# Performance work log

Hardware: AMD Instinct MI355X
Metric: run time of the kernel (lower is better)

The kernel has to match this reference:

```python
import jax, jax.numpy as jnp
import numpy as np
import math

N = 262144   # total points
D = 256      # FEATURE_DIM
B = 16       # batch_size (scenes)

def setup_inputs() -> dict:
    key = jax.random.key(0)
    k0, k1, k2, k3 = jax.random.split(key, 4)
    point_features = jax.random.normal(k0, (N, D), dtype=jnp.float32)
    point_cls_scores = jax.random.uniform(k1, (N,), dtype=jnp.float32)
    # column 0 = sorted batch index in [0, B); remaining columns unused by forward
    bidx = jnp.sort(jax.random.randint(k2, (N,), 0, B, dtype=jnp.int32))
    rest = jax.random.randint(k2, (N, 3), 0, B, dtype=jnp.int32)
    point_coords = jnp.concatenate([bidx[:, None], rest], axis=1)
    # kaiming_uniform_ on (1, D): bound = sqrt(6 / fan_in) with a=sqrt(5) default -> kaiming_uniform_ (no a arg) uses a=0: bound = sqrt(6/D)
    bound = math.sqrt(6.0 / D)
    fc_weight = jax.random.uniform(k3, (1, D), dtype=jnp.float32, minval=-bound, maxval=bound)
    fc_bias = jnp.zeros((1,), dtype=jnp.float32)
    return {
        "point_features": point_features,
        "point_cls_scores": point_cls_scores,
        "point_coords": point_coords,
        "fc_weight": fc_weight,
        "fc_bias": fc_bias,
        "batch_size": B,
    }

def reference(point_features, point_cls_scores, point_coords, fc_weight, fc_bias, batch_size):
    seg = point_coords[:, 0]                                   # [N] int batch ids
    pf = point_features * point_cls_scores[:, None]            # [N, D] scaled features
    sums = jax.ops.segment_sum(pf, seg, num_segments=batch_size)            # [B, D]
    counts = jax.ops.segment_sum(jnp.ones((pf.shape[0],), pf.dtype), seg,
                                 num_segments=batch_size)                   # [B]
    scene_feature = sums / counts[:, None]                     # per-scene mean, [B, D]
    domainness = jax.nn.sigmoid(scene_feature @ fc_weight.T + fc_bias)      # [B, 1]
    return domainness
```

## Files before the change

kernel.cpp:

```cpp
#include <hip/hip_runtime.h>
#include <math.h>

#define NPTS 262144
#define DIM 256
#define NB 16

#define BLOCKS 2048
#define THREADS 256
#define RPB 128
#define WAVES 4
#define ITERS (RPB / WAVES)

__global__ __launch_bounds__(THREADS) void seg_reduce_kernel(
    const float* __restrict__ pf,
    const float* __restrict__ scores,
    const int*   __restrict__ coords,
    float* __restrict__ sums,
    float* __restrict__ counts)
{
    __shared__ float s_score[RPB];
    __shared__ int   s_batch[RPB];
    __shared__ float s_part[WAVES][DIM];

    const int t    = threadIdx.x;
    const int lane = t & 63;
    const int wid  = t >> 6;
    const int col4 = lane << 2;
    const int row0 = blockIdx.x * RPB;

    if (t < RPB) {
        s_score[t] = scores[row0 + t];
        s_batch[t] = coords[(size_t)(row0 + t) * 4];
    }
    __syncthreads();

    const float* base = pf + (size_t)row0 * DIM + col4;

    if (s_batch[0] == s_batch[RPB - 1]) {
        float a0 = 0.f, a1 = 0.f, a2 = 0.f, a3 = 0.f;
        #pragma unroll 8
        for (int it = 0; it < ITERS; ++it) {
            const int r   = (it << 2) + wid;
            const float s = s_score[r];
            const float4 f = *reinterpret_cast<const float4*>(base + (size_t)r * DIM);
            a0 = fmaf(s, f.x, a0);
            a1 = fmaf(s, f.y, a1);
            a2 = fmaf(s, f.z, a2);
            a3 = fmaf(s, f.w, a3);
        }
        float4* dstp = reinterpret_cast<float4*>(&s_part[wid][col4]);
        *dstp = make_float4(a0, a1, a2, a3);
        __syncthreads();
        const int b0 = s_batch[0];
        const float v = s_part[0][t] + s_part[1][t] + s_part[2][t] + s_part[3][t];
        atomicAdd(&sums[(size_t)b0 * DIM + t], v);
        if (t == 0) atomicAdd(&counts[b0], (float)RPB);
    } else {
        float a0 = 0.f, a1 = 0.f, a2 = 0.f, a3 = 0.f;
        float cnt = 0.f;
        int cur_b = -1;
        for (int it = 0; it < ITERS; ++it) {
            const int r   = (it << 2) + wid;
            const int b   = s_batch[r];
            const float s = s_score[r];
            if (b != cur_b) {
                if (cur_b >= 0) {
                    float* dst = sums + (size_t)cur_b * DIM + col4;
                    atomicAdd(dst + 0, a0);
                    atomicAdd(dst + 1, a1);
                    atomicAdd(dst + 2, a2);
                    atomicAdd(dst + 3, a3);
                    if (lane == 0) atomicAdd(counts + cur_b, cnt);
                }
                a0 = a1 = a2 = a3 = 0.f;
                cnt = 0.f;
                cur_b = b;
            }
            const float4 f = *reinterpret_cast<const float4*>(base + (size_t)r * DIM);
            a0 = fmaf(s, f.x, a0);
            a1 = fmaf(s, f.y, a1);
            a2 = fmaf(s, f.z, a2);
            a3 = fmaf(s, f.w, a3);
            cnt += 1.f;
        }
        if (cur_b >= 0) {
            float* dst = sums + (size_t)cur_b * DIM + col4;
            atomicAdd(dst + 0, a0);
            atomicAdd(dst + 1, a1);
            atomicAdd(dst + 2, a2);
            atomicAdd(dst + 3, a3);
            if (lane == 0) atomicAdd(counts + cur_b, cnt);
        }
    }
}

__global__ __launch_bounds__(1024) void head_kernel(
    const float* __restrict__ sums,
    const float* __restrict__ counts,
    const float* __restrict__ w,
    const float* __restrict__ bias,
    float* __restrict__ out)
{
    const int t    = threadIdx.x;
    const int b    = t >> 6;
    const int lane = t & 63;
    const int c    = lane << 2;

    const float inv = 1.f / counts[b];
    const float4 sv = *reinterpret_cast<const float4*>(sums + (size_t)b * DIM + c);
    const float4 wv = *reinterpret_cast<const float4*>(w + c);
    float p = (sv.x * wv.x + sv.y * wv.y + sv.z * wv.z + sv.w * wv.w) * inv;

    #pragma unroll
    for (int off = 32; off > 0; off >>= 1)
        p += __shfl_down(p, off, 64);

    if (lane == 0)
        out[b] = 1.f / (1.f + expf(-(p + bias[0])));
}

extern "C" void kernel_launch(void* const* d_in, const int* in_sizes, int n_in,
                              void* d_out, int out_size, void* d_ws, size_t ws_size,
                              hipStream_t stream) {
    const float* pf      = (const float*)d_in[0];
    const float* scores  = (const float*)d_in[1];
    const int*   coords  = (const int*)d_in[2];
    const float* fc_w    = (const float*)d_in[3];
    const float* fc_b    = (const float*)d_in[4];
    (void)in_sizes; (void)n_in; (void)out_size; (void)ws_size;

    float* sums   = (float*)d_ws;
    float* counts = sums + (size_t)NB * DIM;
    float* out    = (float*)d_out;

    hipMemsetAsync(d_ws, 0, (size_t)(NB * DIM + NB) * sizeof(float), stream);

    seg_reduce_kernel<<<BLOCKS, THREADS, 0, stream>>>(pf, scores, coords, sums, counts);
    head_kernel<<<1, 1024, 0, stream>>>(sums, counts, fc_w, fc_b, out);
}
```

Baseline: 373.8 us.

## Replace uniform-block atomics with per-block partials and a per-scene stage-2 reduction

Blocks whose rows all belong to one scene now write their 256-wide partial sum and scene id to a workspace buffer instead of atomically adding into a shared per-scene sum. A new stage-2 kernel, one block per scene, scans all block ids, sums the matching partials, adds the atomic results from mixed-scene blocks, and applies the linear head and sigmoid. Batch ids are no longer staged in shared memory; only the first and last row ids are loaded, and mixed blocks read coords directly. This removes contention from 2048 blocks hitting 16 rows of atomics, but adds about 2 MB of partial writes and reads plus a serial scan over 2048 ids in each stage-2 block.

```diff
diff --git a/kernel.cpp b/kernel.cpp
--- a/kernel.cpp
+++ b/kernel.cpp
@@ -5,22 +5,25 @@
 #define DIM 256
 #define NB 16
 
-#define BLOCKS 2048
+#define S1_BLOCKS 2048
 #define THREADS 256
-#define RPB 128
+#define RPB (NPTS / S1_BLOCKS)
 #define WAVES 4
 #define ITERS (RPB / WAVES)
 
-__global__ __launch_bounds__(THREADS) void seg_reduce_kernel(
+
+__global__ __launch_bounds__(THREADS) void stage1_kernel(
     const float* __restrict__ pf,
     const float* __restrict__ scores,
     const int*   __restrict__ coords,
-    float* __restrict__ sums,
-    float* __restrict__ counts)
+    float* __restrict__ partials,
+    int*   __restrict__ bids,
+    float* __restrict__ slow_sums,
+    float* __restrict__ slow_counts)
 {
     __shared__ float s_score[RPB];
-    __shared__ int   s_batch[RPB];
     __shared__ float s_part[WAVES][DIM];
+    __shared__ int   s_b0, s_b1;
 
     const int t    = threadIdx.x;
     const int lane = t & 63;
@@ -28,15 +31,14 @@
     const int col4 = lane << 2;
     const int row0 = blockIdx.x * RPB;
 
-    if (t < RPB) {
-        s_score[t] = scores[row0 + t];
-        s_batch[t] = coords[(size_t)(row0 + t) * 4];
-    }
+    if (t < RPB) s_score[t] = scores[row0 + t];
+    if (t == 0)  s_b0 = coords[(size_t)row0 * 4];
+    if (t == 1)  s_b1 = coords[(size_t)(row0 + RPB - 1) * 4];
     __syncthreads();
 
     const float* base = pf + (size_t)row0 * DIM + col4;
 
-    if (s_batch[0] == s_batch[RPB - 1]) {
+    if (s_b0 == s_b1) {
         float a0 = 0.f, a1 = 0.f, a2 = 0.f, a3 = 0.f;
         #pragma unroll 8
         for (int it = 0; it < ITERS; ++it) {
@@ -48,29 +50,28 @@
             a2 = fmaf(s, f.z, a2);
             a3 = fmaf(s, f.w, a3);
         }
-        float4* dstp = reinterpret_cast<float4*>(&s_part[wid][col4]);
-        *dstp = make_float4(a0, a1, a2, a3);
+        *reinterpret_cast<float4*>(&s_part[wid][col4]) = make_float4(a0, a1, a2, a3);
         __syncthreads();
-        const int b0 = s_batch[0];
-        const float v = s_part[0][t] + s_part[1][t] + s_part[2][t] + s_part[3][t];
-        atomicAdd(&sums[(size_t)b0 * DIM + t], v);
-        if (t == 0) atomicAdd(&counts[b0], (float)RPB);
+        partials[(size_t)blockIdx.x * DIM + t] =
+            s_part[0][t] + s_part[1][t] + s_part[2][t] + s_part[3][t];
+        if (t == 0) bids[blockIdx.x] = s_b0;
     } else {
+        if (t == 0) bids[blockIdx.x] = -1;
         float a0 = 0.f, a1 = 0.f, a2 = 0.f, a3 = 0.f;
         float cnt = 0.f;
         int cur_b = -1;
         for (int it = 0; it < ITERS; ++it) {
             const int r   = (it << 2) + wid;
-            const int b   = s_batch[r];
+            const int b   = coords[(size_t)(row0 + r) * 4];
             const float s = s_score[r];
             if (b != cur_b) {
                 if (cur_b >= 0) {
-                    float* dst = sums + (size_t)cur_b * DIM + col4;
+                    float* dst = slow_sums + (size_t)cur_b * DIM + col4;
                     atomicAdd(dst + 0, a0);
                     atomicAdd(dst + 1, a1);
                     atomicAdd(dst + 2, a2);
                     atomicAdd(dst + 3, a3);
-                    if (lane == 0) atomicAdd(counts + cur_b, cnt);
+                    if (lane == 0) atomicAdd(slow_counts + cur_b, cnt);
                 }
                 a0 = a1 = a2 = a3 = 0.f;
                 cnt = 0.f;
@@ -84,39 +85,68 @@
             cnt += 1.f;
         }
         if (cur_b >= 0) {
-            float* dst = sums + (size_t)cur_b * DIM + col4;
+            float* dst = slow_sums + (size_t)cur_b * DIM + col4;
             atomicAdd(dst + 0, a0);
             atomicAdd(dst + 1, a1);
             atomicAdd(dst + 2, a2);
             atomicAdd(dst + 3, a3);
-            if (lane == 0) atomicAdd(counts + cur_b, cnt);
+            if (lane == 0) atomicAdd(slow_counts + cur_b, cnt);
         }
     }
 }
 
-__global__ __launch_bounds__(1024) void head_kernel(
-    const float* __restrict__ sums,
-    const float* __restrict__ counts,
+__global__ __launch_bounds__(THREADS) void stage2_kernel(
+    const float* __restrict__ partials,
+    const int*   __restrict__ bids,
+    const float* __restrict__ slow_sums,
+    const float* __restrict__ slow_counts,
     const float* __restrict__ w,
     const float* __restrict__ bias,
     float* __restrict__ out)
 {
+    __shared__ int   s_bids[S1_BLOCKS];
+    __shared__ float s_part[WAVES][DIM];
+    __shared__ int   s_nm[WAVES];
+    __shared__ float s_red[WAVES];
+
+    const int b    = blockIdx.x;
     const int t    = threadIdx.x;
-    const int b    = t >> 6;
     const int lane = t & 63;
-    const int c    = lane << 2;
+    const int wid  = t >> 6;
+    const int col4 = lane << 2;
 
-    const float inv = 1.f / counts[b];
-    const float4 sv = *reinterpret_cast<const float4*>(sums + (size_t)b * DIM + c);
-    const float4 wv = *reinterpret_cast<const float4*>(w + c);
-    float p = (sv.x * wv.x + sv.y * wv.y + sv.z * wv.z + sv.w * wv.w) * inv;
+    for (int i = t; i < S1_BLOCKS; i += THREADS) s_bids[i] = bids[i];
+    __syncthreads();
 
+    float a0 = 0.f, a1 = 0.f, a2 = 0.f, a3 = 0.f;
+    int nm = 0;
+    for (int blk = wid; blk < S1_BLOCKS; blk += WAVES) {
+        if (s_bids[blk] == b) {
+            const float4 f = *reinterpret_cast<const float4*>(
+                partials + (size_t)blk * DIM + col4);
+            a0 += f.x; a1 += f.y; a2 += f.z; a3 += f.w;
+            ++nm;
+        }
+    }
+    *reinterpret_cast<float4*>(&s_part[wid][col4]) = make_float4(a0, a1, a2, a3);
+    if (lane == 0) s_nm[wid] = nm;
+    __syncthreads();
+
+    const float cnt = (float)RPB * (float)(s_nm[0] + s_nm[1] + s_nm[2] + s_nm[3])
+                      + slow_counts[b];
+    const float v = s_part[0][t] + s_part[1][t] + s_part[2][t] + s_part[3][t]
+                    + slow_sums[(size_t)b * DIM + t];
+
+    float p = (v / cnt) * w[t];
     #pragma unroll
     for (int off = 32; off > 0; off >>= 1)
         p += __shfl_down(p, off, 64);
-
-    if (lane == 0)
-        out[b] = 1.f / (1.f + expf(-(p + bias[0])));
+    if (lane == 0) s_red[wid] = p;
+    __syncthreads();
+    if (t == 0) {
+        const float P = s_red[0] + s_red[1] + s_red[2] + s_red[3] + bias[0];
+        out[b] = 1.f / (1.f + expf(-P));
+    }
 }
 
 extern "C" void kernel_launch(void* const* d_in, const int* in_sizes, int n_in,
@@ -129,12 +159,16 @@
     const float* fc_b    = (const float*)d_in[4];
     (void)in_sizes; (void)n_in; (void)out_size; (void)ws_size;
 
-    float* sums   = (float*)d_ws;
-    float* counts = sums + (size_t)NB * DIM;
-    float* out    = (float*)d_out;
+    float* partials    = (float*)d_ws;
+    int*   bids        = (int*)(partials + (size_t)S1_BLOCKS * DIM);
+    float* slow_sums   = (float*)(bids + S1_BLOCKS);
+    float* slow_counts = slow_sums + (size_t)NB * DIM;
+    float* out         = (float*)d_out;
 
-    hipMemsetAsync(d_ws, 0, (size_t)(NB * DIM + NB) * sizeof(float), stream);
+    hipMemsetAsync(slow_sums, 0, (size_t)(NB * DIM + NB) * sizeof(float), stream);
 
-    seg_reduce_kernel<<<BLOCKS, THREADS, 0, stream>>>(pf, scores, coords, sums, counts);
-    head_kernel<<<1, 1024, 0, stream>>>(sums, counts, fc_w, fc_b, out);
+    stage1_kernel<<<S1_BLOCKS, THREADS, 0, stream>>>(
+        pf, scores, coords, partials, bids, slow_sums, slow_counts);
+    stage2_kernel<<<NB, THREADS, 0, stream>>>(
+        partials, bids, slow_sums, slow_counts, fc_w, fc_b, out);
 }
```

New measurement: 416.2 us. 11.3% more time.
